# Performance work log

Hardware: AMD Instinct MI355X
Metric: run time of the kernel (lower is better)

Reference implementation:

```python
import jax, jax.numpy as jnp
import numpy as np

B, LTMS, TTS, C_IN, F, H = 64, 16, 256, 128, 256, 256


def setup_inputs() -> dict:
    key = jax.random.key(0)
    ks = jax.random.split(key, 6)
    s = 0.05  # small init keeps relu-GRU numerically tame
    return {
        "x": jax.random.normal(ks[0], (B, LTMS * TTS, C_IN), dtype=jnp.float32),
        "conv_w": jax.random.normal(ks[1], (1, C_IN, F), dtype=jnp.float32) * s,
        "conv_b": jnp.zeros((F,), dtype=jnp.float32),
        "attn_w": jax.random.normal(ks[2], (TTS, TTS), dtype=jnp.float32) * s,
        "attn_b": jnp.zeros((TTS,), dtype=jnp.float32),
        "gru_w": jax.random.normal(ks[3], (F, 3 * H), dtype=jnp.float32) * s,
        "gru_u": jax.random.normal(ks[4], (H, 3 * H), dtype=jnp.float32) * s,
        "gru_b": jnp.zeros((2, 3 * H), dtype=jnp.float32),
    }


def _forward(x, conv_w, conv_b, attn_w, attn_b, gru_w, gru_u, gru_b):
    b = x.shape[0]
    # [B, LTMS*TTS, C] -> [B*LTMS, TTS, C]; segments are independent, so the
    # original per-segment Python loop vectorizes into the leading batch dim.
    xs = x.reshape(b * LTMS, TTS, C_IN)
    # Conv1D kernel_size=1 == pointwise GEMM, then ReLU (dropout=0 at inference)
    conv = jax.nn.relu(jnp.einsum('ntc,cf->ntf', xs, conv_w[0]) + conv_b)  # [N,T,F]
    # Attention: softmax(Dense) over time axis per filter, multiply back
    xt = conv.transpose(0, 2, 1)                                  # [N,F,T]
    probs = jax.nn.softmax(xt @ attn_w + attn_b, axis=-1)         # [N,F,T]
    x_att = conv * probs.transpose(0, 2, 1)                       # [N,T,F]
    # GRU (keras v2, reset_after=True), activation=relu, gate order z,r,h
    bi, br = gru_b[0], gru_b[1]
    gates_x = x_att @ gru_w + bi                                  # [N,T,3H]
    def step(h, gx):
        rec = h @ gru_u + br
        xz, xr, xh = jnp.split(gx, 3, axis=-1)
        rz, rr, rh = jnp.split(rec, 3, axis=-1)
        z = jax.nn.sigmoid(xz + rz)
        r = jax.nn.sigmoid(xr + rr)
        hh = jax.nn.relu(xh + r * rh)
        h_new = z * h + (1.0 - z) * hh
        return h_new, None
    h0 = jnp.zeros((b * LTMS, H), dtype=x.dtype)
    h_final, _ = jax.lax.scan(step, h0, gates_x.transpose(1, 0, 2))
    return h_final.reshape(b, LTMS, H)


def reference(x, conv_w, conv_b, attn_w, attn_b, gru_w, gru_u, gru_b):
    return _forward(x, conv_w, conv_b, attn_w, attn_b, gru_w, gru_u, gru_b)
```

## Files before the change

### kernel.cpp

```cpp
#include <hip/hip_runtime.h>
#include <stdint.h>

typedef unsigned short u16;
typedef __attribute__((ext_vector_type(8))) __bf16 bf16x8;
typedef __attribute__((ext_vector_type(4))) float f32x4;

#define TTS 256
#define NSEG 1024
#define TC 32

__device__ __forceinline__ u16 f2bf(float f) {
  union { float f; uint32_t u; } v; v.f = f;
  uint32_t r = v.u + 0x7fffu + ((v.u >> 16) & 1u);
  return (u16)(r >> 16);
}
__device__ __forceinline__ float bf2f(u16 h) {
  union { uint32_t u; float f; } v; v.u = ((uint32_t)h) << 16;
  return v.f;
}
__device__ __forceinline__ float sigm(float x) {
  return __builtin_amdgcn_rcpf(1.0f + __expf(-x));
}

__global__ void k_transp(const float* __restrict__ in, u16* __restrict__ out, int R, int C) {
  int i = blockIdx.x * blockDim.x + threadIdx.x;
  if (i < R * C) {
    int r = i / C, c = i % C;
    out[(size_t)c * R + r] = f2bf(in[i]);
  }
}

template <bool RELU, bool STORE_T, int AMODE>
__global__ __launch_bounds__(256) void k_gemm(
    const void* __restrict__ Av, const u16* __restrict__ Bt,
    const float* __restrict__ bias, u16* __restrict__ out, int K, int Nld, int t0) {
  __shared__ u16 ldsA[4096];
  __shared__ u16 ldsB[4096];
  const int tid  = threadIdx.x;
  const int w    = tid >> 6;
  const int lane = tid & 63;
  const int quad = lane >> 4;
  const int l16  = lane & 15;
  const int m0 = blockIdx.x * 128;
  const int n0 = blockIdx.y * 128;
  const int wm = w >> 1, wn = w & 1;
  const int srow = tid & 127, shalf = tid >> 7;

  f32x4 acc[4][4];
#pragma unroll
  for (int i = 0; i < 4; i++)
#pragma unroll
    for (int j = 0; j < 4; j++) acc[i][j] = f32x4{0.f, 0.f, 0.f, 0.f};

  for (int k0 = 0; k0 < K; k0 += 32) {
    ushort4 va[2][2]; bf16x8 vb[2];
#pragma unroll
    for (int q = 0; q < 2; q++) {
      int c = shalf * 2 + q;
      int kk = k0 + c * 8;
      if (AMODE == 0) {
        const float* Af = (const float*)Av;
        float4 f0 = *(const float4*)(Af + (size_t)(m0 + srow) * K + kk);
        float4 f1 = *(const float4*)(Af + (size_t)(m0 + srow) * K + kk + 4);
        va[q][0] = ushort4{f2bf(f0.x), f2bf(f0.y), f2bf(f0.z), f2bf(f0.w)};
        va[q][1] = ushort4{f2bf(f1.x), f2bf(f1.y), f2bf(f1.z), f2bf(f1.w)};
      } else {
        const u16* Ax = (const u16*)Av;
        int r = m0 + srow;
        const bf16x8 v = *(const bf16x8*)(Ax + (size_t)(r >> 5) * 65536 +
                          (size_t)(kk >> 6) * 16384 + (t0 + (r & 31)) * 64 + (kk & 63));
        va[q][0] = ((const ushort4*)&v)[0];
        va[q][1] = ((const ushort4*)&v)[1];
      }
      vb[q] = *(const bf16x8*)(Bt + (size_t)(n0 + srow) * K + kk);
    }
    __syncthreads();
#pragma unroll
    for (int q = 0; q < 2; q++) {
      int c = shalf * 2 + q;
      *(ushort4*)&ldsA[(c * 128 + srow) * 8]     = va[q][0];
      *(ushort4*)&ldsA[(c * 128 + srow) * 8 + 4] = va[q][1];
      *(bf16x8*)&ldsB[(c * 128 + srow) * 8] = vb[q];
    }
    __syncthreads();
    bf16x8 a[4], b[4];
#pragma unroll
    for (int i = 0; i < 4; i++)
      a[i] = *(const bf16x8*)&ldsA[(quad * 128 + wm * 64 + i * 16 + l16) * 8];
#pragma unroll
    for (int j = 0; j < 4; j++)
      b[j] = *(const bf16x8*)&ldsB[(quad * 128 + wn * 64 + j * 16 + l16) * 8];
#pragma unroll
    for (int i = 0; i < 4; i++)
#pragma unroll
      for (int j = 0; j < 4; j++)
        acc[i][j] = __builtin_amdgcn_mfma_f32_16x16x32_bf16(a[i], b[j], acc[i][j], 0, 0, 0);
  }

#pragma unroll
  for (int j = 0; j < 4; j++) {
    int col = n0 + wn * 64 + j * 16 + l16;
    float bv = bias[col];
#pragma unroll
    for (int i = 0; i < 4; i++) {
      int row0 = m0 + wm * 64 + i * 16 + quad * 4;
      if (STORE_T) {
        int nseg = row0 >> 8, tt0 = row0 & 255;
        ushort4 o;
        float v0 = acc[i][j][0] + bv, v1 = acc[i][j][1] + bv;
        float v2 = acc[i][j][2] + bv, v3 = acc[i][j][3] + bv;
        if (RELU) {
          v0 = fmaxf(v0, 0.f); v1 = fmaxf(v1, 0.f);
          v2 = fmaxf(v2, 0.f); v3 = fmaxf(v3, 0.f);
        }
        o.x = f2bf(v0); o.y = f2bf(v1); o.z = f2bf(v2); o.w = f2bf(v3);
        *(ushort4*)&out[(size_t)nseg * 65536 + (size_t)(col >> 6) * 16384 +
                        (col & 63) * 256 + tt0] = o;
      } else {
#pragma unroll
        for (int r = 0; r < 4; r++) {
          float v = acc[i][j][r] + bv;
          if (RELU) v = fmaxf(v, 0.f);
          out[(size_t)(row0 + r) * Nld + col] = f2bf(v);
        }
      }
    }
  }
}

__global__ __launch_bounds__(256) void k_attn(
    u16* xac,
    const u16* __restrict__ Wt,
    const float* __restrict__ attn_b) {
  __shared__ u16 ldsW[8192];
  __shared__ u16 ldsC[16384];
  __shared__ float redmax[4][64];
  __shared__ float redsum[4][64];
  const int tid  = threadIdx.x;
  const int w    = tid >> 6;
  const int lane = tid & 63;
  const int quad = lane >> 4;
  const int l16  = lane & 15;
  const int seg = blockIdx.x;
  const int c4  = blockIdx.y;
  u16* reg = xac + (size_t)seg * 65536 + (size_t)c4 * 16384;

  {
    const int f = tid & 63, g = tid >> 6;
#pragma unroll
    for (int u = 0; u < 8; u++) {
      int tch = g * 8 + u;
      *(bf16x8*)&ldsC[(tch * 64 + f) * 8] =
          *(const bf16x8*)(reg + (size_t)f * 256 + tch * 8);
    }
  }

  f32x4 acc[4][4];
#pragma unroll
  for (int i = 0; i < 4; i++)
#pragma unroll
    for (int j = 0; j < 4; j++) acc[i][j] = f32x4{0.f, 0.f, 0.f, 0.f};

  for (int s = 0; s < 8; s++) {
    int k0 = s * 32;
    bf16x8 vw[4];
#pragma unroll
    for (int c = 0; c < 4; c++)
      vw[c] = *(const bf16x8*)(Wt + (size_t)tid * 256 + k0 + c * 8);
    __syncthreads();
#pragma unroll
    for (int c = 0; c < 4; c++)
      *(bf16x8*)&ldsW[(c * 256 + tid) * 8] = vw[c];
    __syncthreads();
    bf16x8 a[4], b[4];
#pragma unroll
    for (int i = 0; i < 4; i++)
      a[i] = *(const bf16x8*)&ldsW[(quad * 256 + w * 64 + i * 16 + l16) * 8];
#pragma unroll
    for (int j = 0; j < 4; j++)
      b[j] = *(const bf16x8*)&ldsC[((s * 4 + quad) * 64 + j * 16 + l16) * 8];
#pragma unroll
    for (int i = 0; i < 4; i++)
#pragma unroll
      for (int j = 0; j < 4; j++)
        acc[i][j] = __builtin_amdgcn_mfma_f32_16x16x32_bf16(a[i], b[j], acc[i][j], 0, 0, 0);
  }

#pragma unroll
  for (int i = 0; i < 4; i++)
#pragma unroll
    for (int r = 0; r < 4; r++) {
      float ab = attn_b[w * 64 + i * 16 + quad * 4 + r];
#pragma unroll
      for (int j = 0; j < 4; j++) acc[i][j][r] += ab;
    }

  float lmax[4];
#pragma unroll
  for (int j = 0; j < 4; j++) {
    float m = -1e30f;
#pragma unroll
    for (int i = 0; i < 4; i++)
#pragma unroll
      for (int r = 0; r < 4; r++) m = fmaxf(m, acc[i][j][r]);
    m = fmaxf(m, __shfl_xor(m, 16));
    m = fmaxf(m, __shfl_xor(m, 32));
    lmax[j] = m;
  }
  __syncthreads();
  if (quad == 0) {
#pragma unroll
    for (int j = 0; j < 4; j++) redmax[w][j * 16 + l16] = lmax[j];
  }
  __syncthreads();
  float gmax[4];
#pragma unroll
  for (int j = 0; j < 4; j++) {
    int c = j * 16 + l16;
    gmax[j] = fmaxf(fmaxf(redmax[0][c], redmax[1][c]), fmaxf(redmax[2][c], redmax[3][c]));
  }
  float lsum[4];
#pragma unroll
  for (int j = 0; j < 4; j++) {
    float sacc = 0.f;
#pragma unroll
    for (int i = 0; i < 4; i++)
#pragma unroll
      for (int r = 0; r < 4; r++) {
        float e = __expf(acc[i][j][r] - gmax[j]);
        acc[i][j][r] = e;
        sacc += e;
      }
    sacc += __shfl_xor(sacc, 16);
    sacc += __shfl_xor(sacc, 32);
    lsum[j] = sacc;
  }
  if (quad == 0) {
#pragma unroll
    for (int j = 0; j < 4; j++) redsum[w][j * 16 + l16] = lsum[j];
  }
  __syncthreads();
  float rinv[4];
#pragma unroll
  for (int j = 0; j < 4; j++) {
    int c = j * 16 + l16;
    rinv[j] = 1.0f / (redsum[0][c] + redsum[1][c] + redsum[2][c] + redsum[3][c]);
  }

#pragma unroll
  for (int i = 0; i < 4; i++) {
#pragma unroll
    for (int r = 0; r < 4; r++) {
      int tp = w * 64 + i * 16 + quad * 4 + r;
#pragma unroll
      for (int j = 0; j < 4; j++) {
        int fl = j * 16 + l16;
        float cv = bf2f(ldsC[((tp >> 3) * 64 + fl) * 8 + (tp & 7)]);
        float xa = acc[i][j][r] * rinv[j] * cv;
        reg[(size_t)tp * 64 + fl] = f2bf(xa);
      }
    }
  }
}

__global__ __launch_bounds__(512, 2) void k_scanc(
    const u16* __restrict__ gc,
    const u16* __restrict__ Ut,
    const float* __restrict__ br,
    float* __restrict__ hio,
    int init) {
  __shared__ u16 uls[65536];
  __shared__ u16 hb[16 * 264];
  const int tid  = threadIdx.x;
  const int w    = tid >> 6;
  const int lane = tid & 63;
  const int quad = lane >> 4;
  const int l16  = lane & 15;
  const int n0 = blockIdx.x * 16;
  const int cg[2] = {w, 8 + w};

#pragma unroll
  for (int j = 0; j < 2; j++)
#pragma unroll
    for (int s = 0; s < 8; s++)
      *(bf16x8*)&uls[w * 8192 + (j * 8 + s) * 512 + lane * 8] =
          *(const bf16x8*)(Ut + (size_t)(j * 256 + cg[1] * 16 + l16) * 256 + s * 32 + quad * 8);

  bf16x8 ur0[3][8], urh1[8];
#pragma unroll
  for (int g = 0; g < 3; g++)
#pragma unroll
    for (int s = 0; s < 8; s++)
      ur0[g][s] = *(const bf16x8*)(Ut + (size_t)(g * 256 + cg[0] * 16 + l16) * 256 + s * 32 + quad * 8);
#pragma unroll
  for (int s = 0; s < 8; s++)
    urh1[s] = *(const bf16x8*)(Ut + (size_t)(512 + cg[1] * 16 + l16) * 256 + s * 32 + quad * 8);

  float brZ[2], brR[2], brH[2];
#pragma unroll
  for (int grp = 0; grp < 2; grp++) {
    int c = cg[grp] * 16 + l16;
    brZ[grp] = br[c]; brR[grp] = br[256 + c]; brH[grp] = br[512 + c];
  }

  float hreg[2][4];
#pragma unroll
  for (int grp = 0; grp < 2; grp++)
#pragma unroll
    for (int r = 0; r < 4; r++)
      hreg[grp][r] = init ? 0.f
                          : hio[(size_t)(n0 + quad * 4 + r) * 256 + cg[grp] * 16 + l16];
  {
    int sg = tid >> 5, c0 = (tid & 31) * 8;
    if (init) {
      *(ushort4*)&hb[sg * 264 + c0]     = ushort4{0, 0, 0, 0};
      *(ushort4*)&hb[sg * 264 + c0 + 4] = ushort4{0, 0, 0, 0};
    } else {
      const float* hp = hio + (size_t)(n0 + sg) * 256 + c0;
      float4 h0 = *(const float4*)(hp), h1 = *(const float4*)(hp + 4);
      *(ushort4*)&hb[sg * 264 + c0]     = ushort4{f2bf(h0.x), f2bf(h0.y), f2bf(h0.z), f2bf(h0.w)};
      *(ushort4*)&hb[sg * 264 + c0 + 4] = ushort4{f2bf(h1.x), f2bf(h1.y), f2bf(h1.z), f2bf(h1.w)};
    }
  }
  const u16* gseg[4];
#pragma unroll
  for (int r = 0; r < 4; r++)
    gseg[r] = gc + (size_t)(n0 + quad * 4 + r) * TC * 768;
  __syncthreads();

  for (int tt = 0; tt < TC; tt++) {
    float gg[2][3][4];
#pragma unroll
    for (int grp = 0; grp < 2; grp++)
#pragma unroll
      for (int g = 0; g < 3; g++)
#pragma unroll
        for (int r = 0; r < 4; r++)
          gg[grp][g][r] = bf2f(gseg[r][tt * 768 + g * 256 + cg[grp] * 16 + l16]);

    f32x4 acc[2][3];
#pragma unroll
    for (int grp = 0; grp < 2; grp++)
#pragma unroll
      for (int g = 0; g < 3; g++) acc[grp][g] = f32x4{0.f, 0.f, 0.f, 0.f};

#pragma unroll
    for (int s = 0; s < 8; s++) {
      bf16x8 ah = *(const bf16x8*)&hb[l16 * 264 + s * 32 + quad * 8];
#pragma unroll
      for (int g = 0; g < 3; g++)
        acc[0][g] = __builtin_amdgcn_mfma_f32_16x16x32_bf16(ah, ur0[g][s], acc[0][g], 0, 0, 0);
      bf16x8 uz = *(const bf16x8*)&uls[w * 8192 + s * 512 + lane * 8];
      bf16x8 urr = *(const bf16x8*)&uls[w * 8192 + (8 + s) * 512 + lane * 8];
      acc[1][0] = __builtin_amdgcn_mfma_f32_16x16x32_bf16(ah, uz,      acc[1][0], 0, 0, 0);
      acc[1][1] = __builtin_amdgcn_mfma_f32_16x16x32_bf16(ah, urr,     acc[1][1], 0, 0, 0);
      acc[1][2] = __builtin_amdgcn_mfma_f32_16x16x32_bf16(ah, urh1[s], acc[1][2], 0, 0, 0);
    }
    __syncthreads();

#pragma unroll
    for (int grp = 0; grp < 2; grp++)
#pragma unroll
      for (int r = 0; r < 4; r++) {
        float z  = sigm(acc[grp][0][r] + gg[grp][0][r] + brZ[grp]);
        float rg = sigm(acc[grp][1][r] + gg[grp][1][r] + brR[grp]);
        float hh = fmaxf(gg[grp][2][r] + rg * (acc[grp][2][r] + brH[grp]), 0.f);
        float hn = z * hreg[grp][r] + (1.0f - z) * hh;
        hreg[grp][r] = hn;
        hb[(quad * 4 + r) * 264 + cg[grp] * 16 + l16] = f2bf(hn);
      }
    __syncthreads();
  }

#pragma unroll
  for (int grp = 0; grp < 2; grp++)
#pragma unroll
    for (int r = 0; r < 4; r++)
      hio[(size_t)(n0 + quad * 4 + r) * 256 + cg[grp] * 16 + l16] = hreg[grp][r];
}

extern "C" void kernel_launch(void* const* d_in, const int* in_sizes, int n_in,
                              void* d_out, int out_size, void* d_ws, size_t ws_size,
                              hipStream_t stream) {
  (void)in_sizes; (void)n_in; (void)out_size;
  const float* x      = (const float*)d_in[0];
  const float* conv_w = (const float*)d_in[1];
  const float* conv_b = (const float*)d_in[2];
  const float* attn_w = (const float*)d_in[3];
  const float* attn_b = (const float*)d_in[4];
  const float* gru_w  = (const float*)d_in[5];
  const float* gru_u  = (const float*)d_in[6];
  const float* gru_b  = (const float*)d_in[7];

  const size_t NEEDED = 185532416;
  if (ws_size < NEEDED) return;
  char* ws = (char*)d_ws;
  u16* xac     = (u16*)(ws);
  u16* gatesC  = (u16*)(ws + 134217728);
  u16* conv_wT = (u16*)(ws + 184549376);
  u16* attn_wT = (u16*)(ws + 184614912);
  u16* gru_wT  = (u16*)(ws + 184745984);
  u16* gru_uT  = (u16*)(ws + 185139200);

  hipLaunchKernelGGL(k_transp, dim3(128), dim3(256), 0, stream, conv_w, conv_wT, 128, 256);
  hipLaunchKernelGGL(k_transp, dim3(256), dim3(256), 0, stream, attn_w, attn_wT, 256, 256);
  hipLaunchKernelGGL(k_transp, dim3(768), dim3(256), 0, stream, gru_w, gru_wT, 256, 768);
  hipLaunchKernelGGL(k_transp, dim3(768), dim3(256), 0, stream, gru_u, gru_uT, 256, 768);

  hipLaunchKernelGGL((k_gemm<true, true, 0>), dim3(2048, 2), dim3(256), 0, stream,
                     (const void*)x, conv_wT, conv_b, xac, 128, 0, 0);
  hipLaunchKernelGGL(k_attn, dim3(1024, 4), dim3(256), 0, stream,
                     xac, attn_wT, attn_b);
  for (int c = 0; c < 8; c++) {
    hipLaunchKernelGGL((k_gemm<false, false, 1>), dim3(256, 6), dim3(256), 0, stream,
                       (const void*)xac, gru_wT, gru_b, gatesC, 256, 768, c * TC);
    hipLaunchKernelGGL(k_scanc, dim3(64), dim3(512), 0, stream,
                       gatesC, gru_uT, gru_b + 768, (float*)d_out, c == 0 ? 1 : 0);
  }
}
```

Measured before the change: 1.259 ms.

## Keep attention weights in registers and stream GRU recurrent weights from global

```diff
diff --git a/kernel.cpp b/kernel.cpp
--- a/kernel.cpp
+++ b/kernel.cpp
@@ -132,7 +132,6 @@
     u16* xac,
     const u16* __restrict__ Wt,
     const float* __restrict__ attn_b) {
-  __shared__ u16 ldsW[8192];
   __shared__ u16 ldsC[16384];
   __shared__ float redmax[4][64];
   __shared__ float redsum[4][64];
@@ -145,6 +144,14 @@
   const int c4  = blockIdx.y;
   u16* reg = xac + (size_t)seg * 65536 + (size_t)c4 * 16384;
 
+  bf16x8 wfrag[4][8];
+#pragma unroll
+  for (int i = 0; i < 4; i++)
+#pragma unroll
+    for (int s = 0; s < 8; s++)
+      wfrag[i][s] = *(const bf16x8*)(Wt + (size_t)(w * 64 + i * 16 + l16) * 256 +
+                                     s * 32 + quad * 8);
+
   {
     const int f = tid & 63, g = tid >> 6;
 #pragma unroll
@@ -154,6 +161,7 @@
           *(const bf16x8*)(reg + (size_t)f * 256 + tch * 8);
     }
   }
+  __syncthreads();
 
   f32x4 acc[4][4];
 #pragma unroll
@@ -161,21 +169,9 @@
 #pragma unroll
     for (int j = 0; j < 4; j++) acc[i][j] = f32x4{0.f, 0.f, 0.f, 0.f};
 
+#pragma unroll
   for (int s = 0; s < 8; s++) {
-    int k0 = s * 32;
-    bf16x8 vw[4];
-#pragma unroll
-    for (int c = 0; c < 4; c++)
-      vw[c] = *(const bf16x8*)(Wt + (size_t)tid * 256 + k0 + c * 8);
-    __syncthreads();
-#pragma unroll
-    for (int c = 0; c < 4; c++)
-      *(bf16x8*)&ldsW[(c * 256 + tid) * 8] = vw[c];
-    __syncthreads();
-    bf16x8 a[4], b[4];
-#pragma unroll
-    for (int i = 0; i < 4; i++)
-      a[i] = *(const bf16x8*)&ldsW[(quad * 256 + w * 64 + i * 16 + l16) * 8];
+    bf16x8 b[4];
 #pragma unroll
     for (int j = 0; j < 4; j++)
       b[j] = *(const bf16x8*)&ldsC[((s * 4 + quad) * 64 + j * 16 + l16) * 8];
@@ -183,7 +179,7 @@
     for (int i = 0; i < 4; i++)
 #pragma unroll
       for (int j = 0; j < 4; j++)
-        acc[i][j] = __builtin_amdgcn_mfma_f32_16x16x32_bf16(a[i], b[j], acc[i][j], 0, 0, 0);
+        acc[i][j] = __builtin_amdgcn_mfma_f32_16x16x32_bf16(wfrag[i][s], b[j], acc[i][j], 0, 0, 0);
   }
 
 #pragma unroll
@@ -207,7 +203,6 @@
     m = fmaxf(m, __shfl_xor(m, 32));
     lmax[j] = m;
   }
-  __syncthreads();
   if (quad == 0) {
 #pragma unroll
     for (int j = 0; j < 4; j++) redmax[w][j * 16 + l16] = lmax[j];
@@ -269,7 +264,6 @@
     const float* __restrict__ br,
     float* __restrict__ hio,
     int init) {
-  __shared__ u16 uls[65536];
   __shared__ u16 hb[16 * 264];
   const int tid  = threadIdx.x;
   const int w    = tid >> 6;
@@ -277,39 +271,37 @@
   const int quad = lane >> 4;
   const int l16  = lane & 15;
   const int n0 = blockIdx.x * 16;
-  const int cg[2] = {w, 8 + w};
-
-#pragma unroll
-  for (int j = 0; j < 2; j++)
+  const int cg0 = w, cg1 = 8 + w;
+
+  bf16x8 ur0[3][8], urh1[8];
+#pragma unroll
+  for (int g = 0; g < 3; g++)
 #pragma unroll
     for (int s = 0; s < 8; s++)
-      *(bf16x8*)&uls[w * 8192 + (j * 8 + s) * 512 + lane * 8] =
-          *(const bf16x8*)(Ut + (size_t)(j * 256 + cg[1] * 16 + l16) * 256 + s * 32 + quad * 8);
-
-  bf16x8 ur0[3][8], urh1[8];
-#pragma unroll
-  for (int g = 0; g < 3; g++)
-#pragma unroll
-    for (int s = 0; s < 8; s++)
-      ur0[g][s] = *(const bf16x8*)(Ut + (size_t)(g * 256 + cg[0] * 16 + l16) * 256 + s * 32 + quad * 8);
+      ur0[g][s] = *(const bf16x8*)(Ut + (size_t)(g * 256 + cg0 * 16 + l16) * 256 + s * 32 + quad * 8);
 #pragma unroll
   for (int s = 0; s < 8; s++)
-    urh1[s] = *(const bf16x8*)(Ut + (size_t)(512 + cg[1] * 16 + l16) * 256 + s * 32 + quad * 8);
+    urh1[s] = *(const bf16x8*)(Ut + (size_t)(512 + cg1 * 16 + l16) * 256 + s * 32 + quad * 8);
+
+  const u16* pz1 = Ut + (size_t)(cg1 * 16 + l16) * 256 + quad * 8;
+  const u16* pr1 = Ut + (size_t)(256 + cg1 * 16 + l16) * 256 + quad * 8;
 
   float brZ[2], brR[2], brH[2];
-#pragma unroll
-  for (int grp = 0; grp < 2; grp++) {
-    int c = cg[grp] * 16 + l16;
-    brZ[grp] = br[c]; brR[grp] = br[256 + c]; brH[grp] = br[512 + c];
+  {
+    int c0 = cg0 * 16 + l16, c1 = cg1 * 16 + l16;
+    brZ[0] = br[c0];       brZ[1] = br[c1];
+    brR[0] = br[256 + c0]; brR[1] = br[256 + c1];
+    brH[0] = br[512 + c0]; brH[1] = br[512 + c1];
   }
 
   float hreg[2][4];
 #pragma unroll
   for (int grp = 0; grp < 2; grp++)
 #pragma unroll
-    for (int r = 0; r < 4; r++)
-      hreg[grp][r] = init ? 0.f
-                          : hio[(size_t)(n0 + quad * 4 + r) * 256 + cg[grp] * 16 + l16];
+    for (int r = 0; r < 4; r++) {
+      int c = (grp ? cg1 : cg0) * 16 + l16;
+      hreg[grp][r] = init ? 0.f : hio[(size_t)(n0 + quad * 4 + r) * 256 + c];
+    }
   {
     int sg = tid >> 5, c0 = (tid & 31) * 8;
     if (init) {
@@ -335,8 +327,17 @@
 #pragma unroll
       for (int g = 0; g < 3; g++)
 #pragma unroll
-        for (int r = 0; r < 4; r++)
-          gg[grp][g][r] = bf2f(gseg[r][tt * 768 + g * 256 + cg[grp] * 16 + l16]);
+        for (int r = 0; r < 4; r++) {
+          int c = (grp ? cg1 : cg0) * 16 + l16;
+          gg[grp][g][r] = bf2f(gseg[r][tt * 768 + g * 256 + c]);
+        }
+
+    bf16x8 uz1[4], ur1[4];
+#pragma unroll
+    for (int s = 0; s < 4; s++) {
+      uz1[s] = *(const bf16x8*)(pz1 + s * 32);
+      ur1[s] = *(const bf16x8*)(pr1 + s * 32);
+    }
 
     f32x4 acc[2][3];
 #pragma unroll
@@ -350,11 +351,13 @@
 #pragma unroll
       for (int g = 0; g < 3; g++)
         acc[0][g] = __builtin_amdgcn_mfma_f32_16x16x32_bf16(ah, ur0[g][s], acc[0][g], 0, 0, 0);
-      bf16x8 uz = *(const bf16x8*)&uls[w * 8192 + s * 512 + lane * 8];
-      bf16x8 urr = *(const bf16x8*)&uls[w * 8192 + (8 + s) * 512 + lane * 8];
-      acc[1][0] = __builtin_amdgcn_mfma_f32_16x16x32_bf16(ah, uz,      acc[1][0], 0, 0, 0);
-      acc[1][1] = __builtin_amdgcn_mfma_f32_16x16x32_bf16(ah, urr,     acc[1][1], 0, 0, 0);
-      acc[1][2] = __builtin_amdgcn_mfma_f32_16x16x32_bf16(ah, urh1[s], acc[1][2], 0, 0, 0);
+      acc[1][0] = __builtin_amdgcn_mfma_f32_16x16x32_bf16(ah, uz1[s & 3],  acc[1][0], 0, 0, 0);
+      acc[1][1] = __builtin_amdgcn_mfma_f32_16x16x32_bf16(ah, ur1[s & 3],  acc[1][1], 0, 0, 0);
+      acc[1][2] = __builtin_amdgcn_mfma_f32_16x16x32_bf16(ah, urh1[s],     acc[1][2], 0, 0, 0);
+      if (s < 4) {
+        uz1[s] = *(const bf16x8*)(pz1 + (s + 4) * 32);
+        ur1[s] = *(const bf16x8*)(pr1 + (s + 4) * 32);
+      }
     }
     __syncthreads();
 
@@ -362,12 +365,13 @@
     for (int grp = 0; grp < 2; grp++)
 #pragma unroll
       for (int r = 0; r < 4; r++) {
+        int c = (grp ? cg1 : cg0) * 16 + l16;
         float z  = sigm(acc[grp][0][r] + gg[grp][0][r] + brZ[grp]);
         float rg = sigm(acc[grp][1][r] + gg[grp][1][r] + brR[grp]);
         float hh = fmaxf(gg[grp][2][r] + rg * (acc[grp][2][r] + brH[grp]), 0.f);
         float hn = z * hreg[grp][r] + (1.0f - z) * hh;
         hreg[grp][r] = hn;
-        hb[(quad * 4 + r) * 264 + cg[grp] * 16 + l16] = f2bf(hn);
+        hb[(quad * 4 + r) * 264 + c] = f2bf(hn);
       }
     __syncthreads();
   }
@@ -375,8 +379,10 @@
 #pragma unroll
   for (int grp = 0; grp < 2; grp++)
 #pragma unroll
-    for (int r = 0; r < 4; r++)
-      hio[(size_t)(n0 + quad * 4 + r) * 256 + cg[grp] * 16 + l16] = hreg[grp][r];
+    for (int r = 0; r < 4; r++) {
+      int c = (grp ? cg1 : cg0) * 16 + l16;
+      hio[(size_t)(n0 + quad * 4 + r) * 256 + c] = hreg[grp][r];
+    }
 }
 
 extern "C" void kernel_launch(void* const* d_in, const int* in_sizes, int n_in,
```

Result: slower. 1.797 ms (+42.8%).
